# Kernel tuning notes

Measured on AMD Instinct MI355X. Metric: run time of the kernel, lower is better.

Reference implementation:

```python
import jax, jax.numpy as jnp
import numpy as np

KS = [3, 3, 7, 7, 11, 11, 21, 21]  # TEXT_KERNEL_SIZES
KMAX = 21
H = 8
D_MODEL = 1024
D_H = D_MODEL // H
R = 4
B = 2
N = 4096


def _extract_windows_1d(xh, k):
    # xh: (B, n, d_h) -> windows: (B, n, k, d_h), zero-padded, stride 1
    pad = k // 2
    xp = jnp.pad(xh, ((0, 0), (pad, pad), (0, 0)))
    idx = jnp.arange(xh.shape[1])[:, None] + jnp.arange(k)[None, :]  # (n, k)
    return xp[:, idx]  # (B, n, k, d_h)


def setup_inputs() -> dict:
    key = jax.random.key(0)
    ks = jax.random.split(key, 10)
    s = 0.02
    return {
        "x": jax.random.normal(ks[0], (B, N, D_MODEL), dtype=jnp.float32),
        "W_in": jax.random.normal(ks[1], (D_MODEL, D_MODEL), dtype=jnp.float32) * s,
        "b_in": jnp.zeros((D_MODEL,), dtype=jnp.float32),
        "W_out": jax.random.normal(ks[2], (D_MODEL, D_MODEL), dtype=jnp.float32) * (0.02 / np.sqrt(2.0 * 8)),
        "b_out": jnp.zeros((D_MODEL,), dtype=jnp.float32),
        "Wc": jax.random.normal(ks[3], (H, D_H, R), dtype=jnp.float32) * s,  # per-token coeff proj
        "A": jax.random.normal(ks[4], (H, R, KMAX), dtype=jnp.float32) * s,  # rank -> kernel-pos factor (padded to KMAX)
        "V": jax.random.normal(ks[5], (H, R, D_H), dtype=jnp.float32) * s,   # rank -> channel factor
        "base": jax.random.normal(ks[6], (H, KMAX, D_H), dtype=jnp.float32) * s,  # static kernel (padded)
        "alphas": jnp.zeros((H,), dtype=jnp.float32),  # sigmoid gate params
    }


def reference(x, W_in, b_in, W_out, b_out, Wc, A, V, base, alphas):
    Bsz, n, d = x.shape
    x_proj = x @ W_in.T + b_in                        # (B, n, d_model)
    x_heads = x_proj.reshape(Bsz, n, H, D_H)          # (B, n, H, d_h)
    head_outs = []
    for h in range(H):
        k = KS[h]
        x_h = x_heads[:, :, h, :]                     # (B, n, d_h)
        # Factored per-token kernel generation
        c = x_h @ Wc[h]                               # (B, n, R)
        dyn = jnp.einsum('bnr,rk,rd->bnkd', c, A[h, :, :k], V[h])  # (B, n, k, d_h)
        alpha = jax.nn.sigmoid(alphas[h])
        K_hat = alpha * dyn + (1.0 - alpha) * base[h, :k][None, None]  # (B, n, k, d_h)
        windows = _extract_windows_1d(x_h, k)         # (B, n, k, d_h)
        o_h = jnp.einsum('bnkd,bnkd->bnd', K_hat, windows)
        head_outs.append(o_h)
    concat = jnp.concatenate(head_outs, axis=-1)      # (B, n, d_model)
    return concat @ W_out.T + b_out
```

## Files before the change

kernel.cpp:

```cpp
#include <hip/hip_runtime.h>
#include <stdint.h>

typedef __bf16 bf16;
typedef __bf16 bf16x8 __attribute__((ext_vector_type(8)));
typedef float f32x4 __attribute__((ext_vector_type(4)));

#define AS1 __attribute__((address_space(1)))
#define AS3 __attribute__((address_space(3)))

__device__ __forceinline__ void gload_lds16(const void* g, void* l) {
    __builtin_amdgcn_global_load_lds((const AS1 uint32_t*)g, (AS3 uint32_t*)l, 16, 0, 0);
}

#define BM 128
#define BN 64
#define BK 64

template <typename OT>
__global__ __launch_bounds__(256, 4) void gemm_nt(
    const bf16* __restrict__ A, const bf16* __restrict__ B,
    const float* __restrict__ bias, OT* __restrict__ C,
    int M, int N, int K)
{
    __shared__ bf16 smA[BM * BK];
    __shared__ bf16 smB[BN * BK];

    const int tid  = threadIdx.x;
    const int wave = tid >> 6;
    const int lane = tid & 63;
    const int wm = (wave >> 1) * 64;
    const int wn = (wave & 1) * 32;
    const int rowA0 = blockIdx.x * BM;
    const int rowB0 = blockIdx.y * BN;

    f32x4 acc[4][2] = {};

    const int g  = lane >> 4;
    const int rm = lane & 15;

    for (int k0 = 0; k0 < K; k0 += BK) {
        #pragma unroll
        for (int i = 0; i < 4; ++i) {
            int slot = i * 256 + tid;
            int row  = slot >> 3;
            int kg   = slot & 7;
            int kd   = kg ^ ((row >> 1) & 7);
            gload_lds16(A + (size_t)(rowA0 + row) * K + k0 + kd * 8, &smA[slot * 8]);
        }
        #pragma unroll
        for (int i = 0; i < 2; ++i) {
            int slot = i * 256 + tid;
            int row  = slot >> 3;
            int kg   = slot & 7;
            int kd   = kg ^ ((row >> 1) & 7);
            gload_lds16(B + (size_t)(rowB0 + row) * K + k0 + kd * 8, &smB[slot * 8]);
        }
        __syncthreads();

        #pragma unroll
        for (int s = 0; s < 2; ++s) {
            bf16x8 af[4], bfr[2];
            #pragma unroll
            for (int mi = 0; mi < 4; ++mi) {
                int row  = wm + mi * 16 + rm;
                int slot = row * 8 + ((s * 4 + g) ^ ((row >> 1) & 7));
                af[mi] = *(const bf16x8*)&smA[slot * 8];
            }
            #pragma unroll
            for (int ni = 0; ni < 2; ++ni) {
                int row  = wn + ni * 16 + rm;
                int slot = row * 8 + ((s * 4 + g) ^ ((row >> 1) & 7));
                bfr[ni] = *(const bf16x8*)&smB[slot * 8];
            }
            #pragma unroll
            for (int mi = 0; mi < 4; ++mi)
                #pragma unroll
                for (int ni = 0; ni < 2; ++ni)
                    acc[mi][ni] = __builtin_amdgcn_mfma_f32_16x16x32_bf16(
                        af[mi], bfr[ni], acc[mi][ni], 0, 0, 0);
        }
        __syncthreads();
    }

    const int quad = lane >> 4;
    #pragma unroll
    for (int ni = 0; ni < 2; ++ni) {
        int col = rowB0 + wn + ni * 16 + rm;
        float bcol = bias[col];
        #pragma unroll
        for (int mi = 0; mi < 4; ++mi) {
            #pragma unroll
            for (int r = 0; r < 4; ++r) {
                int rowc = rowA0 + wm + mi * 16 + quad * 4 + r;
                C[(size_t)rowc * N + col] = (OT)(acc[mi][ni][r] + bcol);
            }
        }
    }
}

__global__ void cast_all_kernel(const float* __restrict__ x, bf16* __restrict__ xb,
                                const float* __restrict__ wi, bf16* __restrict__ wib,
                                const float* __restrict__ wo, bf16* __restrict__ wob)
{
    const int NX8 = (2 * 4096 * 1024) / 8;
    const int NW8 = (1024 * 1024) / 8;
    int i = blockIdx.x * 256 + threadIdx.x;
    const float* in; bf16* out; int idx;
    if (i < NX8)            { in = x;  out = xb;  idx = i; }
    else if (i < NX8 + NW8) { in = wi; out = wib; idx = i - NX8; }
    else                    { in = wo; out = wob; idx = i - NX8 - NW8; }
    const float4* p = (const float4*)in;
    float4 a = p[2 * idx], b = p[2 * idx + 1];
    bf16x8 o;
    o[0] = (bf16)a.x; o[1] = (bf16)a.y; o[2] = (bf16)a.z; o[3] = (bf16)a.w;
    o[4] = (bf16)b.x; o[5] = (bf16)b.y; o[6] = (bf16)b.z; o[7] = (bf16)b.w;
    *(bf16x8*)(out + 8 * idx) = o;
}

__global__ __launch_bounds__(256) void c_compute(
    const bf16* __restrict__ xpb, const float* __restrict__ Wc,
    float* __restrict__ cbuf)
{
    const int wave = threadIdx.x >> 6, lane = threadIdx.x & 63;
    const int row  = blockIdx.x * 4 + wave;
    const int h    = lane >> 3;
    const int d0   = (lane & 7) * 16;

    const bf16* xr = xpb + (size_t)row * 1024 + lane * 16;
    bf16x8 v0 = *(const bf16x8*)xr;
    bf16x8 v1 = *(const bf16x8*)(xr + 8);
    float p0 = 0.f, p1 = 0.f, p2 = 0.f, p3 = 0.f;
    #pragma unroll
    for (int i = 0; i < 16; ++i) {
        float xv = (i < 8) ? (float)v0[i & 7] : (float)v1[i & 7];
        float4 wr = *(const float4*)(Wc + h * 512 + (d0 + i) * 4);
        p0 += xv * wr.x; p1 += xv * wr.y; p2 += xv * wr.z; p3 += xv * wr.w;
    }
    #pragma unroll
    for (int off = 1; off <= 4; off <<= 1) {
        p0 += __shfl_xor(p0, off);
        p1 += __shfl_xor(p1, off);
        p2 += __shfl_xor(p2, off);
        p3 += __shfl_xor(p3, off);
    }
    if ((lane & 7) == 0) {
        float4 o = {p0, p1, p2, p3};
        *(float4*)(cbuf + (size_t)row * 32 + h * 4) = o;
    }
}

__constant__ int KS_c[8] = {3, 3, 7, 7, 11, 11, 21, 21};

template <int K>
__device__ __forceinline__ void mix_body3(
    int h, int tid, int r0, const bf16* __restrict__ xpb,
    const float* __restrict__ cbuf, const float* __restrict__ Aw,
    const float* __restrict__ Vw, const float* __restrict__ basew,
    float alpha, bf16* __restrict__ y, bf16* sx)
{
    constexpr int T   = 8;
    constexpr int pad = K / 2;
    constexpr int R   = 16 + 2 * pad;
    constexpr int S   = R * 16;
    constexpr int NP  = (S + 255) / 256;

    #pragma unroll
    for (int p = 0; p < NP; ++p) {
        int slot = p * 256 + tid;
        if (slot < S) {
            int lrow = slot >> 4;
            int lc   = slot & 15;
            int grow = r0 - pad + lrow;
            grow = min(max(grow, 0), 8191);
            gload_lds16(xpb + (size_t)grow * 1024 + h * 128 + lc * 8,
                        sx + slot * 8);
        }
    }
    __syncthreads();

    const int d   = tid & 127;
    const int sub = tid >> 7;
    const int lr0 = sub * 8;
    const int nb  = (r0 & 4095) + sub * 8;

    float w[T + K - 1];
    #pragma unroll
    for (int j = 0; j < T + K - 1; ++j) {
        int nl = nb + j - pad;
        float v = (float)sx[(lr0 + j) * 128 + d];
        w[j] = (nl >= 0 && nl < 4096) ? v : 0.f;
    }

    float s0[T] = {}, s1[T] = {}, s2[T] = {}, s3[T] = {}, tv[T] = {};
    const float* Ah = Aw + h * 84;
    const float* bh = basew + h * 2688 + d;
    #pragma unroll
    for (int j = 0; j < K; ++j) {
        float a0 = Ah[j], a1 = Ah[21 + j], a2 = Ah[42 + j], a3 = Ah[63 + j];
        float bbj = bh[j * 128];
        #pragma unroll
        for (int t = 0; t < T; ++t) {
            float x = w[t + j];
            s0[t] += a0 * x; s1[t] += a1 * x;
            s2[t] += a2 * x; s3[t] += a3 * x;
            tv[t] += bbj * x;
        }
    }

    float v0 = Vw[h * 512 + d],       v1 = Vw[h * 512 + 128 + d];
    float v2 = Vw[h * 512 + 256 + d], v3 = Vw[h * 512 + 384 + d];
    #pragma unroll
    for (int t = 0; t < T; ++t) {
        int rowo = r0 + sub * 8 + t;
        float4 c4 = *(const float4*)(cbuf + (size_t)rowo * 32 + h * 4);
        float o = alpha * (c4.x * v0 * s0[t] + c4.y * v1 * s1[t] +
                           c4.z * v2 * s2[t] + c4.w * v3 * s3[t])
                + (1.f - alpha) * tv[t];
        y[(size_t)rowo * 1024 + h * 128 + d] = (bf16)o;
    }
}

__global__ __launch_bounds__(256, 4) void head_mix3(
    const bf16* __restrict__ xpb, const float* __restrict__ cbuf,
    const float* __restrict__ Aw, const float* __restrict__ Vw,
    const float* __restrict__ basew, const float* __restrict__ alphas,
    bf16* __restrict__ y)
{
    __shared__ bf16 sx[36 * 128];
    const int h  = blockIdx.y;
    const int r0 = blockIdx.x * 16;
    const float alpha = 1.f / (1.f + __expf(-alphas[h]));

    switch (KS_c[h]) {
        case 3:  mix_body3<3 >(h, threadIdx.x, r0, xpb, cbuf, Aw, Vw, basew, alpha, y, sx); break;
        case 7:  mix_body3<7 >(h, threadIdx.x, r0, xpb, cbuf, Aw, Vw, basew, alpha, y, sx); break;
        case 11: mix_body3<11>(h, threadIdx.x, r0, xpb, cbuf, Aw, Vw, basew, alpha, y, sx); break;
        default: mix_body3<21>(h, threadIdx.x, r0, xpb, cbuf, Aw, Vw, basew, alpha, y, sx); break;
    }
}

extern "C" void kernel_launch(void* const* d_in, const int* in_sizes, int n_in,
                              void* d_out, int out_size, void* d_ws, size_t ws_size,
                              hipStream_t stream)
{
    const float* x      = (const float*)d_in[0];
    const float* W_in   = (const float*)d_in[1];
    const float* b_in   = (const float*)d_in[2];
    const float* W_out  = (const float*)d_in[3];
    const float* b_out  = (const float*)d_in[4];
    const float* Wc     = (const float*)d_in[5];
    const float* Aw     = (const float*)d_in[6];
    const float* Vw     = (const float*)d_in[7];
    const float* basew  = (const float*)d_in[8];
    const float* alphas = (const float*)d_in[9];
    float* out = (float*)d_out;

    const size_t MB = 1u << 20;
    char* ws = (char*)d_ws;
    bf16*  xb   = (bf16*) (ws);
    bf16*  wib  = (bf16*) (ws + 16 * MB);
    bf16*  wob  = (bf16*) (ws + 18 * MB);
    bf16*  xpb  = (bf16*) (ws + 20 * MB);
    bf16*  yb   = (bf16*) (ws + 36 * MB);
    float* cbuf = (float*)(ws + 52 * MB);

    const int NTOT8 = (2 * 4096 * 1024 + 2 * 1024 * 1024) / 8;

    cast_all_kernel<<<NTOT8 / 256, 256, 0, stream>>>(x, xb, W_in, wib, W_out, wob);

    gemm_nt<bf16><<<dim3(8192 / BM, 1024 / BN), 256, 0, stream>>>(
        xb, wib, b_in, xpb, 8192, 1024, 1024);

    c_compute<<<8192 / 4, 256, 0, stream>>>(xpb, Wc, cbuf);

    head_mix3<<<dim3(512, 8), 256, 0, stream>>>(
        xpb, cbuf, Aw, Vw, basew, alphas, yb);

    gemm_nt<float><<<dim3(8192 / BM, 1024 / BN), 256, 0, stream>>>(
        yb, wob, b_out, out, 8192, 1024, 1024);
}
```

Measured before the change: 178.4 us.

## Fuse per-token coefficient projection into head mixing kernel and stage weights in LDS

Removes the separate c_compute kernel and its global cbuf round trip by computing the rank-4 coefficients inside the head-mix block from the already-loaded LDS tile, using wave-wide shuffle reductions. Base, V and A weights are now staged into shared memory with async global-to-LDS loads, and the rank loop is restructured to accumulate one rank at a time to lower register pressure. This saves a kernel launch and an extra read of xpb. In exchange it adds LDS use (around 13KB more per block), which may reduce occupancy, plus an extra barrier and a full 64-lane shuffle reduction per row.

```diff
diff --git a/kernel.cpp b/kernel.cpp
--- a/kernel.cpp
+++ b/kernel.cpp
@@ -117,125 +117,137 @@
     *(bf16x8*)(out + 8 * idx) = o;
 }
 
-__global__ __launch_bounds__(256) void c_compute(
-    const bf16* __restrict__ xpb, const float* __restrict__ Wc,
-    float* __restrict__ cbuf)
-{
-    const int wave = threadIdx.x >> 6, lane = threadIdx.x & 63;
-    const int row  = blockIdx.x * 4 + wave;
-    const int h    = lane >> 3;
-    const int d0   = (lane & 7) * 16;
-
-    const bf16* xr = xpb + (size_t)row * 1024 + lane * 16;
-    bf16x8 v0 = *(const bf16x8*)xr;
-    bf16x8 v1 = *(const bf16x8*)(xr + 8);
-    float p0 = 0.f, p1 = 0.f, p2 = 0.f, p3 = 0.f;
-    #pragma unroll
-    for (int i = 0; i < 16; ++i) {
-        float xv = (i < 8) ? (float)v0[i & 7] : (float)v1[i & 7];
-        float4 wr = *(const float4*)(Wc + h * 512 + (d0 + i) * 4);
-        p0 += xv * wr.x; p1 += xv * wr.y; p2 += xv * wr.z; p3 += xv * wr.w;
-    }
-    #pragma unroll
-    for (int off = 1; off <= 4; off <<= 1) {
-        p0 += __shfl_xor(p0, off);
-        p1 += __shfl_xor(p1, off);
-        p2 += __shfl_xor(p2, off);
-        p3 += __shfl_xor(p3, off);
-    }
-    if ((lane & 7) == 0) {
-        float4 o = {p0, p1, p2, p3};
-        *(float4*)(cbuf + (size_t)row * 32 + h * 4) = o;
-    }
-}
-
 __constant__ int KS_c[8] = {3, 3, 7, 7, 11, 11, 21, 21};
 
 template <int K>
-__device__ __forceinline__ void mix_body3(
+__device__ __forceinline__ void mix_body4(
     int h, int tid, int r0, const bf16* __restrict__ xpb,
-    const float* __restrict__ cbuf, const float* __restrict__ Aw,
+    const float* __restrict__ Wc, const float* __restrict__ Aw,
     const float* __restrict__ Vw, const float* __restrict__ basew,
-    float alpha, bf16* __restrict__ y, bf16* sx)
+    float alpha, bf16* __restrict__ y,
+    bf16* sx, float* sB, float* sV, float* sA, float* sc)
 {
     constexpr int T   = 8;
     constexpr int pad = K / 2;
     constexpr int R   = 16 + 2 * pad;
-    constexpr int S   = R * 16;
-    constexpr int NP  = (S + 255) / 256;
-
-    #pragma unroll
-    for (int p = 0; p < NP; ++p) {
+    constexpr int SX  = R * 16;
+    constexpr int SB  = K * 32;
+
+    #pragma unroll
+    for (int p = 0; p < (SX + 255) / 256; ++p) {
         int slot = p * 256 + tid;
-        if (slot < S) {
+        if (slot < SX) {
             int lrow = slot >> 4;
-            int lc   = slot & 15;
-            int grow = r0 - pad + lrow;
-            grow = min(max(grow, 0), 8191);
-            gload_lds16(xpb + (size_t)grow * 1024 + h * 128 + lc * 8,
+            int grow = min(max(r0 - pad + lrow, 0), 8191);
+            gload_lds16(xpb + (size_t)grow * 1024 + h * 128 + (slot & 15) * 8,
                         sx + slot * 8);
+        }
+    }
+    #pragma unroll
+    for (int p = 0; p < (SB + 255) / 256; ++p) {
+        int slot = p * 256 + tid;
+        if (slot < SB)
+            gload_lds16(basew + h * 2688 + slot * 4, sB + slot * 4);
+    }
+    if (tid < 128) gload_lds16(Vw + h * 512 + tid * 4, sV + tid * 4);
+    if (tid < 21)  gload_lds16(Aw + h * 84 + tid * 4, sA + tid * 4);
+    __syncthreads();
+
+    {
+        const int wv = tid >> 6, lane = tid & 63;
+        #pragma unroll
+        for (int q = 0; q < 4; ++q) {
+            int lrow = pad + wv * 4 + q;
+            float x0 = (float)sx[lrow * 128 + lane];
+            float x1 = (float)sx[lrow * 128 + 64 + lane];
+            float4 w0 = *(const float4*)(Wc + h * 512 + lane * 4);
+            float4 w1 = *(const float4*)(Wc + h * 512 + (64 + lane) * 4);
+            float p0 = x0 * w0.x + x1 * w1.x;
+            float p1 = x0 * w0.y + x1 * w1.y;
+            float p2 = x0 * w0.z + x1 * w1.z;
+            float p3 = x0 * w0.w + x1 * w1.w;
+            #pragma unroll
+            for (int off = 1; off < 64; off <<= 1) {
+                p0 += __shfl_xor(p0, off);
+                p1 += __shfl_xor(p1, off);
+                p2 += __shfl_xor(p2, off);
+                p3 += __shfl_xor(p3, off);
+            }
+            if (lane == 0) {
+                sc[(wv * 4 + q) * 4 + 0] = p0;
+                sc[(wv * 4 + q) * 4 + 1] = p1;
+                sc[(wv * 4 + q) * 4 + 2] = p2;
+                sc[(wv * 4 + q) * 4 + 3] = p3;
+            }
         }
     }
     __syncthreads();
 
     const int d   = tid & 127;
     const int sub = tid >> 7;
-    const int lr0 = sub * 8;
     const int nb  = (r0 & 4095) + sub * 8;
 
     float w[T + K - 1];
     #pragma unroll
     for (int j = 0; j < T + K - 1; ++j) {
         int nl = nb + j - pad;
-        float v = (float)sx[(lr0 + j) * 128 + d];
+        float v = (float)sx[(sub * 8 + j) * 128 + d];
         w[j] = (nl >= 0 && nl < 4096) ? v : 0.f;
     }
 
-    float s0[T] = {}, s1[T] = {}, s2[T] = {}, s3[T] = {}, tv[T] = {};
-    const float* Ah = Aw + h * 84;
-    const float* bh = basew + h * 2688 + d;
+    float o[T] = {};
+    #pragma unroll
+    for (int r = 0; r < 4; ++r) {
+        float s[T] = {};
+        #pragma unroll
+        for (int j = 0; j < K; ++j) {
+            float a = sA[r * 21 + j];
+            #pragma unroll
+            for (int t = 0; t < T; ++t) s[t] += a * w[t + j];
+        }
+        float vr = sV[r * 128 + d];
+        #pragma unroll
+        for (int t = 0; t < T; ++t)
+            o[t] += (sc[(sub * 8 + t) * 4 + r] * vr) * s[t];
+    }
+
+    float tv[T] = {};
     #pragma unroll
     for (int j = 0; j < K; ++j) {
-        float a0 = Ah[j], a1 = Ah[21 + j], a2 = Ah[42 + j], a3 = Ah[63 + j];
-        float bbj = bh[j * 128];
-        #pragma unroll
-        for (int t = 0; t < T; ++t) {
-            float x = w[t + j];
-            s0[t] += a0 * x; s1[t] += a1 * x;
-            s2[t] += a2 * x; s3[t] += a3 * x;
-            tv[t] += bbj * x;
-        }
-    }
-
-    float v0 = Vw[h * 512 + d],       v1 = Vw[h * 512 + 128 + d];
-    float v2 = Vw[h * 512 + 256 + d], v3 = Vw[h * 512 + 384 + d];
+        float bb = sB[j * 128 + d];
+        #pragma unroll
+        for (int t = 0; t < T; ++t) tv[t] += bb * w[t + j];
+    }
+
     #pragma unroll
     for (int t = 0; t < T; ++t) {
         int rowo = r0 + sub * 8 + t;
-        float4 c4 = *(const float4*)(cbuf + (size_t)rowo * 32 + h * 4);
-        float o = alpha * (c4.x * v0 * s0[t] + c4.y * v1 * s1[t] +
-                           c4.z * v2 * s2[t] + c4.w * v3 * s3[t])
-                + (1.f - alpha) * tv[t];
-        y[(size_t)rowo * 1024 + h * 128 + d] = (bf16)o;
-    }
-}
-
-__global__ __launch_bounds__(256, 4) void head_mix3(
-    const bf16* __restrict__ xpb, const float* __restrict__ cbuf,
+        float res = alpha * o[t] + (1.f - alpha) * tv[t];
+        y[(size_t)rowo * 1024 + h * 128 + d] = (bf16)res;
+    }
+}
+
+__global__ __launch_bounds__(256, 4) void head_mix4(
+    const bf16* __restrict__ xpb, const float* __restrict__ Wc,
     const float* __restrict__ Aw, const float* __restrict__ Vw,
     const float* __restrict__ basew, const float* __restrict__ alphas,
     bf16* __restrict__ y)
 {
-    __shared__ bf16 sx[36 * 128];
+    __shared__ __align__(16) bf16  sx[36 * 128];
+    __shared__ __align__(16) float sB[21 * 128];
+    __shared__ __align__(16) float sV[512];
+    __shared__ __align__(16) float sA[84];
+    __shared__ float sc[16 * 4];
+
     const int h  = blockIdx.y;
     const int r0 = blockIdx.x * 16;
     const float alpha = 1.f / (1.f + __expf(-alphas[h]));
 
     switch (KS_c[h]) {
-        case 3:  mix_body3<3 >(h, threadIdx.x, r0, xpb, cbuf, Aw, Vw, basew, alpha, y, sx); break;
-        case 7:  mix_body3<7 >(h, threadIdx.x, r0, xpb, cbuf, Aw, Vw, basew, alpha, y, sx); break;
-        case 11: mix_body3<11>(h, threadIdx.x, r0, xpb, cbuf, Aw, Vw, basew, alpha, y, sx); break;
-        default: mix_body3<21>(h, threadIdx.x, r0, xpb, cbuf, Aw, Vw, basew, alpha, y, sx); break;
+        case 3:  mix_body4<3 >(h, threadIdx.x, r0, xpb, Wc, Aw, Vw, basew, alpha, y, sx, sB, sV, sA, sc); break;
+        case 7:  mix_body4<7 >(h, threadIdx.x, r0, xpb, Wc, Aw, Vw, basew, alpha, y, sx, sB, sV, sA, sc); break;
+        case 11: mix_body4<11>(h, threadIdx.x, r0, xpb, Wc, Aw, Vw, basew, alpha, y, sx, sB, sV, sA, sc); break;
+        default: mix_body4<21>(h, threadIdx.x, r0, xpb, Wc, Aw, Vw, basew, alpha, y, sx, sB, sV, sA, sc); break;
     }
 }
 
@@ -262,7 +274,6 @@
     bf16*  wob  = (bf16*) (ws + 18 * MB);
     bf16*  xpb  = (bf16*) (ws + 20 * MB);
     bf16*  yb   = (bf16*) (ws + 36 * MB);
-    float* cbuf = (float*)(ws + 52 * MB);
 
     const int NTOT8 = (2 * 4096 * 1024 + 2 * 1024 * 1024) / 8;
 
@@ -271,10 +282,8 @@
     gemm_nt<bf16><<<dim3(8192 / BM, 1024 / BN), 256, 0, stream>>>(
         xb, wib, b_in, xpb, 8192, 1024, 1024);
 
-    c_compute<<<8192 / 4, 256, 0, stream>>>(xpb, Wc, cbuf);
-
-    head_mix3<<<dim3(512, 8), 256, 0, stream>>>(
-        xpb, cbuf, Aw, Vw, basew, alphas, yb);
+    head_mix4<<<dim3(512, 8), 256, 0, stream>>>(
+        xpb, Wc, Aw, Vw, basew, alphas, yb);
 
     gemm_nt<float><<<dim3(8192 / BM, 1024 / BN), 256, 0, stream>>>(
         yb, wob, b_out, out, 8192, 1024, 1024);
```

After: 242.1 us. 1.36x slower.
